# Kernel tuning notes

Measured on AMD Instinct MI355X. Metric: run time of the kernel, lower is better.

## Reference

```python
import jax, jax.numpy as jnp
import numpy as np

FEATURE_DIM = 512
HIDDEN_DIM = 512
N_HEADS = 8
HEAD_DIM = HIDDEN_DIM // N_HEADS
MAX_LEN = 5000
GAMMA = 0.5  # gaussian relative-position bias width
LN_EPS = 1e-5


def make_pe(d_model, max_len):
    # sinusoidal positional encoding buffer, as in PositionalEncoding.__init__
    pos = jnp.arange(max_len, dtype=jnp.float32)[:, None]
    div = jnp.exp(jnp.arange(0, d_model, 2, dtype=jnp.float32) * (-np.log(10000.0) / d_model))
    ang = pos * div  # [max_len, d_model/2]
    pe = jnp.zeros((max_len, d_model), dtype=jnp.float32)
    pe = pe.at[:, 0::2].set(jnp.sin(ang)).at[:, 1::2].set(jnp.cos(ang))
    return pe


def setup_inputs() -> dict:
    key = jax.random.key(0)
    k_x, k_q, k_k, k_v = jax.random.split(key, 4)
    xavier = np.sqrt(6.0 / (FEATURE_DIM + HEAD_DIM))  # xavier_uniform over last two dims
    return {
        "data_window": jax.random.normal(k_x, (1, 2048, FEATURE_DIM), dtype=jnp.float32),
        "W_query": jax.random.uniform(k_q, (N_HEADS, FEATURE_DIM, HEAD_DIM), jnp.float32, -xavier, xavier),
        "W_key": jax.random.uniform(k_k, (N_HEADS, FEATURE_DIM, HEAD_DIM), jnp.float32, -xavier, xavier),
        "W_value": jax.random.uniform(k_v, (N_HEADS, FEATURE_DIM, HEAD_DIM), jnp.float32, -xavier, xavier),
        "ln_gamma": jnp.ones((FEATURE_DIM,), dtype=jnp.float32),
        "ln_beta": jnp.zeros((FEATURE_DIM,), dtype=jnp.float32),
    }


def reference(data_window, W_query, W_key, W_value, ln_gamma, ln_beta):
    B, S, F = data_window.shape
    temperature = 1.0

    # LayerNorm over feature dim
    mu = jnp.mean(data_window, axis=-1, keepdims=True)
    var = jnp.mean(jnp.square(data_window - mu), axis=-1, keepdims=True)
    x = (data_window - mu) * jax.lax.rsqrt(var + LN_EPS) * ln_gamma + ln_beta

    # positional encoding, exactly as original: x + pe[:x.shape[0]] (requires B==1)
    pe = make_pe(FEATURE_DIM, MAX_LEN)
    x = x + pe[:B]  # [B,F] broadcasts over [B,S,F] only because B==1

    # per-head QKV projections, vectorized over heads
    Q = jnp.einsum('bsf,hfd->bhsd', x, W_query)
    K = jnp.einsum('bsf,hfd->bhsd', x, W_key)
    V = jnp.einsum('bsf,hfd->bhsd', x, W_value)

    scores = jnp.einsum('bhsd,bhtd->bhst', Q, K) / np.sqrt(HEAD_DIM)

    # gaussian relative-position bias: scale(=1) * exp(-gamma * (i-j)^2)
    p = jnp.arange(S, dtype=jnp.float32)
    rel = p[:, None] - p[None, :]
    bias = jnp.exp(-GAMMA * jnp.square(rel))  # [S,S]
    scores = (scores + bias[None, None]) / temperature
    # dropout on scores is identity in eval mode

    attn = jax.nn.softmax(scores, axis=-1)  # [B,H,S,S]
    head_out = jnp.einsum('bhst,bhtd->bhsd', attn, V)

    # concat heads along feature dim: [B,S,H*D]
    multi_head_output = head_out.transpose(0, 2, 1, 3).reshape(B, S, N_HEADS * HEAD_DIM)
    mean_weights = jnp.mean(attn, axis=1)  # [B,S,S]
    return multi_head_output, mean_weights
```

## Files before the change

kernel.cpp:

```cpp
#include <hip/hip_runtime.h>
#include <hip/hip_bf16.h>
#include <math.h>

#define S_LEN 2048
#define FDIM  512
#define NH    8
#define HD    64
#define MH_ELEMS (S_LEN * FDIM)
#define MEAN_ELEMS (S_LEN * S_LEN)

typedef _Float16 half_t;
typedef _Float16 half2v __attribute__((ext_vector_type(2)));
typedef _Float16 half4v __attribute__((ext_vector_type(4)));
typedef _Float16 half8v __attribute__((ext_vector_type(8)));
typedef float    float4v __attribute__((ext_vector_type(4)));
typedef int      int4v   __attribute__((ext_vector_type(4)));
typedef unsigned short ushort4v __attribute__((ext_vector_type(4)));

#define MFMA16(a, b, c) __builtin_amdgcn_mfma_f32_16x16x32_f16((a), (b), (c), 0, 0, 0)

static __device__ __forceinline__ unsigned short f2bf(float x) {
    union { __hip_bfloat16 b; unsigned short u; } cv;
    cv.b = __float2bfloat16(x);
    return cv.u;
}

__global__ __launch_bounds__(256) void prep_kernel(const float* __restrict__ x,
                                                   const float* __restrict__ gamma,
                                                   const float* __restrict__ beta,
                                                   const float* __restrict__ Wq,
                                                   const float* __restrict__ Wk,
                                                   const float* __restrict__ Wv,
                                                   half_t* __restrict__ xo,
                                                   half_t* __restrict__ WT) {
    const int tid = threadIdx.x;
    if (blockIdx.x < 2048) {
        const int row = blockIdx.x;
        const float2 v = ((const float2*)(x + (size_t)row * FDIM))[tid];
        float s = v.x + v.y;
        float q = v.x * v.x + v.y * v.y;
        #pragma unroll
        for (int off = 1; off < 64; off <<= 1) {
            s += __shfl_xor(s, off, 64);
            q += __shfl_xor(q, off, 64);
        }
        __shared__ float red[8];
        const int wave = tid >> 6;
        if ((tid & 63) == 0) { red[wave] = s; red[4 + wave] = q; }
        __syncthreads();
        s = red[0] + red[1] + red[2] + red[3];
        q = red[4] + red[5] + red[6] + red[7];
        const float mu  = s * (1.0f / FDIM);
        const float var = q * (1.0f / FDIM) - mu * mu;
        const float rstd = rsqrtf(var + 1e-5f);
        const int f0 = tid * 2, f1 = tid * 2 + 1;
        const float o0 = (v.x - mu) * rstd * gamma[f0] + beta[f0];
        const float o1 = (v.y - mu) * rstd * gamma[f1] + beta[f1] + 1.0f;
        half2v o; o.x = (half_t)o0; o.y = (half_t)o1;
        ((half2v*)(xo + (size_t)row * FDIM))[tid] = o;
    } else {
        const int idx = blockIdx.x - 2048;
        const int k0 = (idx & 7) * 64;
        const int h  = (idx >> 3) & 7;
        const int z  = idx >> 6;
        const float* W = ((z == 0) ? Wq : (z == 1) ? Wk : Wv) + (size_t)h * FDIM * HD;
        __shared__ float Ls[64][65];
        {
            const int kk = tid >> 2, dg = (tid & 3) * 16;
            #pragma unroll
            for (int j = 0; j < 4; ++j) {
                const float4 w = *(const float4*)(W + (size_t)(k0 + kk) * HD + dg + j * 4);
                Ls[kk][dg + j * 4 + 0] = w.x; Ls[kk][dg + j * 4 + 1] = w.y;
                Ls[kk][dg + j * 4 + 2] = w.z; Ls[kk][dg + j * 4 + 3] = w.w;
            }
        }
        __syncthreads();
        {
            const int d = tid >> 2, kg = (tid & 3) * 16;
            half8v t0, t1;
            #pragma unroll
            for (int j = 0; j < 8; ++j) t0[j] = (half_t)Ls[kg + j][d];
            #pragma unroll
            for (int j = 0; j < 8; ++j) t1[j] = (half_t)Ls[kg + 8 + j][d];
            half_t* dst = WT + ((size_t)(z * NH + h) * HD + d) * FDIM + k0 + kg;
            *(half8v*)dst = t0;
            *(half8v*)(dst + 8) = t1;
        }
    }
}

__global__ __launch_bounds__(256) void qkv_kernel(const half_t* __restrict__ xh,
                                                  const half_t* __restrict__ WT,
                                                  half_t* __restrict__ Qo,
                                                  half_t* __restrict__ Ko,
                                                  half_t* __restrict__ VTo) {
    const int ms0 = blockIdx.x * 128;
    const int h   = blockIdx.y, z = blockIdx.z;
    const half_t* Wt = WT + (size_t)(z * NH + h) * HD * FDIM;

    const int tid = threadIdx.x;
    const int wv = tid >> 6, lane = tid & 63;
    const int lo = lane & 15, qq = lane >> 4;

    float4v acc[2][4];
    #pragma unroll
    for (int rg = 0; rg < 2; ++rg)
        #pragma unroll
        for (int cg = 0; cg < 4; ++cg) acc[rg][cg] = (float4v){0.f, 0.f, 0.f, 0.f};

    const half_t* ar[2];
    ar[0] = xh + (size_t)(ms0 + wv * 32 + lo) * FDIM + qq * 8;
    ar[1] = ar[0] + 16 * FDIM;
    const half_t* wrow[4];
    #pragma unroll
    for (int cg = 0; cg < 4; ++cg) wrow[cg] = Wt + (size_t)(cg * 16 + lo) * FDIM + qq * 8;

    half8v a_c[2][2], b_c[4][2];
    #pragma unroll
    for (int rg = 0; rg < 2; ++rg) { a_c[rg][0] = *(const half8v*)(ar[rg]); a_c[rg][1] = *(const half8v*)(ar[rg] + 32); }
    #pragma unroll
    for (int cg = 0; cg < 4; ++cg) { b_c[cg][0] = *(const half8v*)(wrow[cg]); b_c[cg][1] = *(const half8v*)(wrow[cg] + 32); }

    for (int k0 = 0; k0 < FDIM; k0 += 64) {
        const int kn0 = (k0 + 64 < FDIM) ? k0 + 64 : 0;
        const int kn1 = (k0 + 96 < FDIM) ? k0 + 96 : 0;
        half8v a_n[2][2], b_n[4][2];
        #pragma unroll
        for (int rg = 0; rg < 2; ++rg) { a_n[rg][0] = *(const half8v*)(ar[rg] + kn0); a_n[rg][1] = *(const half8v*)(ar[rg] + kn1); }
        #pragma unroll
        for (int cg = 0; cg < 4; ++cg) { b_n[cg][0] = *(const half8v*)(wrow[cg] + kn0); b_n[cg][1] = *(const half8v*)(wrow[cg] + kn1); }
        #pragma unroll
        for (int kh = 0; kh < 2; ++kh)
            #pragma unroll
            for (int rg = 0; rg < 2; ++rg)
                #pragma unroll
                for (int cg = 0; cg < 4; ++cg)
                    acc[rg][cg] = MFMA16(a_c[rg][kh], b_c[cg][kh], acc[rg][cg]);
        #pragma unroll
        for (int rg = 0; rg < 2; ++rg) { a_c[rg][0] = a_n[rg][0]; a_c[rg][1] = a_n[rg][1]; }
        #pragma unroll
        for (int cg = 0; cg < 4; ++cg) { b_c[cg][0] = b_n[cg][0]; b_c[cg][1] = b_n[cg][1]; }
    }

    if (z < 2) {
        half_t* Co = ((z == 0) ? Qo : Ko) + (size_t)h * S_LEN * HD;
        #pragma unroll
        for (int rg = 0; rg < 2; ++rg)
            #pragma unroll
            for (int cg = 0; cg < 4; ++cg)
                #pragma unroll
                for (int r = 0; r < 4; ++r)
                    Co[(size_t)(ms0 + wv * 32 + rg * 16 + qq * 4 + r) * HD + cg * 16 + lo] =
                        (half_t)acc[rg][cg][r];
    } else {
        __shared__ float Ls[128][65];
        #pragma unroll
        for (int rg = 0; rg < 2; ++rg)
            #pragma unroll
            for (int cg = 0; cg < 4; ++cg)
                #pragma unroll
                for (int r = 0; r < 4; ++r)
                    Ls[wv * 32 + rg * 16 + qq * 4 + r][cg * 16 + lo] = acc[rg][cg][r];
        __syncthreads();
        const int d = tid & 63, sg = tid >> 6;
        half_t* dst = VTo + (size_t)(h * HD + d) * S_LEN + ms0 + sg * 32;
        #pragma unroll
        for (int c = 0; c < 4; ++c) {
            half8v t;
            #pragma unroll
            for (int j = 0; j < 8; ++j) t[j] = (half_t)Ls[sg * 32 + c * 8 + j][d];
            *(half8v*)(dst + c * 8) = t;
        }
    }
}

__global__ __launch_bounds__(256) void attn2_kernel(const half_t* __restrict__ Qw,
                                                    const half_t* __restrict__ Kw,
                                                    const half_t* __restrict__ VT,
                                                    unsigned short* __restrict__ Praw,
                                                    half_t* __restrict__ Op,
                                                    float* __restrict__ mp,
                                                    float* __restrict__ lp) {
    const int s0 = blockIdx.x * 32;
    const int h  = blockIdx.y;
    const int z  = blockIdx.z;
    const half_t* Qh = Qw + (size_t)h * S_LEN * HD;
    const half_t* Kh = Kw + (size_t)h * S_LEN * HD;
    const half_t* Vt = VT + (size_t)h * (size_t)HD * S_LEN;

    __shared__ float Osh[4][32][65];
    __shared__ float lsh[4][32];
    __shared__ float msh[4][32];

    const int tid = threadIdx.x;
    const int wv = tid >> 6, lane = tid & 63;
    const int lo = lane & 15, qq = lane >> 4;
    const int tb = z * 1024 + wv * 256;

    const half8v qA0 = *(const half8v*)(Qh + (size_t)(s0 + lo) * HD + qq * 8);
    const half8v qA1 = *(const half8v*)(Qh + (size_t)(s0 + lo) * HD + 32 + qq * 8);
    const half8v qB0 = *(const half8v*)(Qh + (size_t)(s0 + 16 + lo) * HD + qq * 8);
    const half8v qB1 = *(const half8v*)(Qh + (size_t)(s0 + 16 + lo) * HD + 32 + qq * 8);

    float4v accA[4], accB[4];
    #pragma unroll
    for (int dt = 0; dt < 4; ++dt) {
        accA[dt] = (float4v){0.f, 0.f, 0.f, 0.f};
        accB[dt] = (float4v){0.f, 0.f, 0.f, 0.f};
    }
    float mA = 0.f, mB = 0.f, lA = 0.f, lB = 0.f;

    const int srcLow  = lo + ((qq & 1) * 2) * 16;
    const int srcHigh = srcLow + 16;
    const bool sel1 = (qq >> 1) != 0;

    unsigned short* prA = Praw + ((size_t)h << 22) + (size_t)(s0 + lo) * S_LEN + qq * 4;
    unsigned short* prB = prA + 16 * S_LEN;

    half8v kc[4];
    {
        const half_t* kp0 = Kh + (size_t)(tb + lo) * HD;
        const half_t* kp1 = Kh + (size_t)(tb + 16 + lo) * HD;
        kc[0] = *(const half8v*)(kp0 + qq * 8);
        kc[1] = *(const half8v*)(kp0 + 32 + qq * 8);
        kc[2] = *(const half8v*)(kp1 + qq * 8);
        kc[3] = *(const half8v*)(kp1 + 32 + qq * 8);
    }

    for (int ps = 0; ps < 8; ++ps) {
        const int Tg  = tb + ps * 32;
        const int Tgn = tb + ((ps < 7) ? ps + 1 : ps) * 32;
        half8v kn[4], vc[4];
        {
            const half_t* kp0 = Kh + (size_t)(Tgn + lo) * HD;
            const half_t* kp1 = Kh + (size_t)(Tgn + 16 + lo) * HD;
            kn[0] = *(const half8v*)(kp0 + qq * 8);
            kn[1] = *(const half8v*)(kp0 + 32 + qq * 8);
            kn[2] = *(const half8v*)(kp1 + qq * 8);
            kn[3] = *(const half8v*)(kp1 + 32 + qq * 8);
            #pragma unroll
            for (int dt = 0; dt < 4; ++dt)
                vc[dt] = *(const half8v*)(Vt + (size_t)(dt * 16 + lo) * S_LEN + Tg + qq * 8);
        }
        float4v c0A = (float4v){0.f, 0.f, 0.f, 0.f};
        c0A = MFMA16(kc[0], qA0, c0A); c0A = MFMA16(kc[1], qA1, c0A);
        float4v c1A = (float4v){0.f, 0.f, 0.f, 0.f};
        c1A = MFMA16(kc[2], qA0, c1A); c1A = MFMA16(kc[3], qA1, c1A);
        float4v c0B = (float4v){0.f, 0.f, 0.f, 0.f};
        c0B = MFMA16(kc[0], qB0, c0B); c0B = MFMA16(kc[1], qB1, c0B);
        float4v c1B = (float4v){0.f, 0.f, 0.f, 0.f};
        c1B = MFMA16(kc[2], qB0, c1B); c1B = MFMA16(kc[3], qB1, c1B);

        const int dd0 = s0 - Tg;
        const bool nA0 = (dd0 > -40) && (dd0 < 40);
        const bool nA1 = (dd0 - 16 > -40) && (dd0 - 16 < 40);
        const bool nB0 = (dd0 + 16 > -40) && (dd0 + 16 < 40);
        const bool nB1 = nA0;
        float S0A[4], S1A[4], S0B[4], S1B[4];
        #pragma unroll
        for (int r = 0; r < 4; ++r) {
            const int t0 = Tg + qq * 4 + r, t1 = t0 + 16;
            float sa0 = c0A[r] * 0.125f;
            if (nA0) { const float d = (float)(s0 + lo - t0); sa0 += __expf(-0.5f * d * d); }
            float sa1 = c1A[r] * 0.125f;
            if (nA1) { const float d = (float)(s0 + lo - t1); sa1 += __expf(-0.5f * d * d); }
            float sb0 = c0B[r] * 0.125f;
            if (nB0) { const float d = (float)(s0 + 16 + lo - t0); sb0 += __expf(-0.5f * d * d); }
            float sb1 = c1B[r] * 0.125f;
            if (nB1) { const float d = (float)(s0 + 16 + lo - t1); sb1 += __expf(-0.5f * d * d); }
            S0A[r] = sa0; S1A[r] = sa1; S0B[r] = sb0; S1B[r] = sb1;
        }
        float smA = fmaxf(fmaxf(fmaxf(S0A[0], S0A[1]), fmaxf(S0A[2], S0A[3])),
                          fmaxf(fmaxf(S1A[0], S1A[1]), fmaxf(S1A[2], S1A[3])));
        float smB = fmaxf(fmaxf(fmaxf(S0B[0], S0B[1]), fmaxf(S0B[2], S0B[3])),
                          fmaxf(fmaxf(S1B[0], S1B[1]), fmaxf(S1B[2], S1B[3])));
        smA = fmaxf(smA, __shfl_xor(smA, 16, 64));
        smA = fmaxf(smA, __shfl_xor(smA, 32, 64));
        smB = fmaxf(smB, __shfl_xor(smB, 16, 64));
        smB = fmaxf(smB, __shfl_xor(smB, 32, 64));
        const float mnA = fmaxf(mA, smA), mnB = fmaxf(mB, smB);
        const float alA = __expf(mA - mnA), alB = __expf(mB - mnB);
        mA = mnA; mB = mnB;
        float E0A[4], E1A[4], E0B[4], E1B[4];
        float lsA = 0.f, lsB = 0.f;
        #pragma unroll
        for (int r = 0; r < 4; ++r) {
            E0A[r] = __expf(S0A[r] - mnA); E1A[r] = __expf(S1A[r] - mnA);
            E0B[r] = __expf(S0B[r] - mnB); E1B[r] = __expf(S1B[r] - mnB);
            lsA += E0A[r] + E1A[r];
            lsB += E0B[r] + E1B[r];
        }
        lA = lA * alA + lsA;
        lB = lB * alB + lsB;
        #pragma unroll
        for (int dt = 0; dt < 4; ++dt)
            #pragma unroll
            for (int i = 0; i < 4; ++i) { accA[dt][i] *= alA; accB[dt][i] *= alB; }

        {
            const float emA = __expf(mnA), emB = __expf(mnB);
            ushort4v e0a, e1a, e0b, e1b;
            #pragma unroll
            for (int r = 0; r < 4; ++r) {
                e0a[r] = f2bf(E0A[r] * emA); e1a[r] = f2bf(E1A[r] * emA);
                e0b[r] = f2bf(E0B[r] * emB); e1b[r] = f2bf(E1B[r] * emB);
            }
            *(ushort4v*)(prA + Tg)      = e0a;
            *(ushort4v*)(prA + Tg + 16) = e1a;
            *(ushort4v*)(prB + Tg)      = e0b;
            *(ushort4v*)(prB + Tg + 16) = e1b;
        }

        int pkA0, pkA1, pkA2, pkA3, pkB0, pkB1, pkB2, pkB3;
        {
            half2v p;
            p.x = (half_t)E0A[0]; p.y = (half_t)E0A[1]; pkA0 = __builtin_bit_cast(int, p);
            p.x = (half_t)E0A[2]; p.y = (half_t)E0A[3]; pkA1 = __builtin_bit_cast(int, p);
            p.x = (half_t)E1A[0]; p.y = (half_t)E1A[1]; pkA2 = __builtin_bit_cast(int, p);
            p.x = (half_t)E1A[2]; p.y = (half_t)E1A[3]; pkA3 = __builtin_bit_cast(int, p);
            p.x = (half_t)E0B[0]; p.y = (half_t)E0B[1]; pkB0 = __builtin_bit_cast(int, p);
            p.x = (half_t)E0B[2]; p.y = (half_t)E0B[3]; pkB1 = __builtin_bit_cast(int, p);
            p.x = (half_t)E1B[0]; p.y = (half_t)E1B[1]; pkB2 = __builtin_bit_cast(int, p);
            p.x = (half_t)E1B[2]; p.y = (half_t)E1B[3]; pkB3 = __builtin_bit_cast(int, p);
        }
        int4v biA, biB;
        {
            const int l0a = __shfl(pkA0, srcLow, 64),  l0b = __shfl(pkA2, srcLow, 64);
            const int l1a = __shfl(pkA1, srcLow, 64),  l1b = __shfl(pkA3, srcLow, 64);
            const int h0a = __shfl(pkA0, srcHigh, 64), h0b = __shfl(pkA2, srcHigh, 64);
            const int h1a = __shfl(pkA1, srcHigh, 64), h1b = __shfl(pkA3, srcHigh, 64);
            biA[0] = sel1 ? l0b : l0a;
            biA[1] = sel1 ? l1b : l1a;
            biA[2] = sel1 ? h0b : h0a;
            biA[3] = sel1 ? h1b : h1a;
        }
        {
            const int l0a = __shfl(pkB0, srcLow, 64),  l0b = __shfl(pkB2, srcLow, 64);
            const int l1a = __shfl(pkB1, srcLow, 64),  l1b = __shfl(pkB3, srcLow, 64);
            const int h0a = __shfl(pkB0, srcHigh, 64), h0b = __shfl(pkB2, srcHigh, 64);
            const int h1a = __shfl(pkB1, srcHigh, 64), h1b = __shfl(pkB3, srcHigh, 64);
            biB[0] = sel1 ? l0b : l0a;
            biB[1] = sel1 ? l1b : l1a;
            biB[2] = sel1 ? h0b : h0a;
            biB[3] = sel1 ? h1b : h1a;
        }
        const half8v bpA = __builtin_bit_cast(half8v, biA);
        const half8v bpB = __builtin_bit_cast(half8v, biB);
        #pragma unroll
        for (int dt = 0; dt < 4; ++dt) {
            accA[dt] = MFMA16(vc[dt], bpA, accA[dt]);
            accB[dt] = MFMA16(vc[dt], bpB, accB[dt]);
        }
        #pragma unroll
        for (int i = 0; i < 4; ++i) kc[i] = kn[i];
    }

    lA += __shfl_xor(lA, 16, 64); lA += __shfl_xor(lA, 32, 64);
    lB += __shfl_xor(lB, 16, 64); lB += __shfl_xor(lB, 32, 64);
    if (qq == 0) {
        lsh[wv][lo] = lA;      msh[wv][lo] = mA;
        lsh[wv][16 + lo] = lB; msh[wv][16 + lo] = mB;
    }
    #pragma unroll
    for (int dt = 0; dt < 4; ++dt)
        #pragma unroll
        for (int r = 0; r < 4; ++r) {
            Osh[wv][lo][dt * 16 + qq * 4 + r]      = accA[dt][r];
            Osh[wv][16 + lo][dt * 16 + qq * 4 + r] = accB[dt][r];
        }
    __syncthreads();

    #pragma unroll
    for (int p = 0; p < 2; ++p) {
        const int q = p * 16 + (tid >> 4), dg = tid & 15;
        const float m0 = msh[0][q], m1 = msh[1][q], m2 = msh[2][q], m3 = msh[3][q];
        const float M = fmaxf(fmaxf(m0, m1), fmaxf(m2, m3));
        const float f0 = __expf(m0 - M), f1 = __expf(m1 - M);
        const float f2 = __expf(m2 - M), f3 = __expf(m3 - M);
        const float L = lsh[0][q] * f0 + lsh[1][q] * f1 + lsh[2][q] * f2 + lsh[3][q] * f3;
        half4v o;
        #pragma unroll
        for (int i = 0; i < 4; ++i) {
            const float ov = Osh[0][q][dg * 4 + i] * f0 + Osh[1][q][dg * 4 + i] * f1 +
                             Osh[2][q][dg * 4 + i] * f2 + Osh[3][q][dg * 4 + i] * f3;
            o[i] = (half_t)ov;
        }
        const size_t pidx = (size_t)(z * NH + h) * S_LEN + s0 + q;
        *(half4v*)(Op + pidx * HD + dg * 4) = o;
        if (dg == 0) { mp[pidx] = M; lp[pidx] = L; }
    }
}

__global__ __launch_bounds__(256) void meanmerge_kernel(const half_t* __restrict__ Op,
                                                        const float* __restrict__ mp,
                                                        const float* __restrict__ lp,
                                                        const unsigned short* __restrict__ Praw,
                                                        float* __restrict__ out) {
    const int q = blockIdx.x;
    const int tid = threadIdx.x;
    __shared__ float lish[NH];
    {
        const int h = tid >> 5, t32 = tid & 31;
        const size_t i0 = (size_t)h * S_LEN + q;
        const size_t i1 = (size_t)(NH + h) * S_LEN + q;
        const float m0 = mp[i0], m1 = mp[i1];
        const float M = fmaxf(m0, m1);
        const float f0 = __expf(m0 - M), f1 = __expf(m1 - M);
        const float L = lp[i0] * f0 + lp[i1] * f1;
        const float inv = 1.0f / L;
        if (t32 == 0) lish[h] = __expf(-M) * inv;
        const int d = t32 * 2;
        const half2v o0 = *(const half2v*)(Op + i0 * HD + d);
        const half2v o1 = *(const half2v*)(Op + i1 * HD + d);
        float2 o;
        o.x = ((float)o0.x * f0 + (float)o1.x * f1) * inv;
        o.y = ((float)o0.y * f0 + (float)o1.y * f1) * inv;
        *(float2*)(out + (size_t)q * FDIM + h * HD + d) = o;
    }
    __syncthreads();
    {
        const int idx = tid * 8;
        float acc[8] = {0.f, 0.f, 0.f, 0.f, 0.f, 0.f, 0.f, 0.f};
        #pragma unroll
        for (int h = 0; h < NH; ++h) {
            const uint4 u = *(const uint4*)(Praw + ((size_t)h << 22) + (size_t)q * S_LEN + idx);
            const float li = lish[h];
            const unsigned int uu[4] = {u.x, u.y, u.z, u.w};
            #pragma unroll
            for (int j = 0; j < 4; ++j) {
                const float a = __builtin_bit_cast(float, uu[j] << 16);
                const float b = __builtin_bit_cast(float, uu[j] & 0xFFFF0000u);
                acc[2 * j]     += a * li;
                acc[2 * j + 1] += b * li;
            }
        }
        float* o = out + MH_ELEMS + (size_t)q * S_LEN + idx;
        *(float4*)o       = make_float4(acc[0] * 0.125f, acc[1] * 0.125f, acc[2] * 0.125f, acc[3] * 0.125f);
        *(float4*)(o + 4) = make_float4(acc[4] * 0.125f, acc[5] * 0.125f, acc[6] * 0.125f, acc[7] * 0.125f);
    }
}

extern "C" void kernel_launch(void* const* d_in, const int* in_sizes, int n_in,
                              void* d_out, int out_size, void* d_ws, size_t ws_size,
                              hipStream_t stream) {
    const float* x  = (const float*)d_in[0];
    const float* Wq = (const float*)d_in[1];
    const float* Wk = (const float*)d_in[2];
    const float* Wv = (const float*)d_in[3];
    const float* g  = (const float*)d_in[4];
    const float* b  = (const float*)d_in[5];
    float* out = (float*)d_out;
    char*  ws  = (char*)d_ws;

    half_t* Qh   = (half_t*)(ws);
    half_t* Kh   = (half_t*)(ws + (2ull  << 20));
    half_t* VT   = (half_t*)(ws + (4ull  << 20));
    half_t* xh   = (half_t*)(ws + (6ull  << 20));
    half_t* WT   = (half_t*)(ws + (8ull  << 20));
    half_t* Op   = (half_t*)(ws + (10ull << 20));
    float*  mp   = (float*) (ws + (14ull << 20));
    float*  lp   = (float*) (ws + (14ull << 20) + (128ull << 10));
    unsigned short* Praw = (unsigned short*)(ws + (16ull << 20));

    prep_kernel<<<2240, 256, 0, stream>>>(x, g, b, Wq, Wk, Wv, xh, WT);
    qkv_kernel<<<dim3(16, 8, 3), 256, 0, stream>>>(xh, WT, Qh, Kh, VT);
    attn2_kernel<<<dim3(64, 8, 2), 256, 0, stream>>>(Qh, Kh, VT, Praw, Op, mp, lp);
    meanmerge_kernel<<<S_LEN, 256, 0, stream>>>(Op, mp, lp, Praw, out);
}
```

Before: 157.5 us.

## Recompute attention probabilities in mean kernel instead of storing bf16 P matrix

The attention kernel no longer writes per-head unnormalized probabilities (8x2048x2048 bf16) to workspace. A new mean kernel recomputes QK^T per head with MFMA and turns each score into a normalized probability using the saved row max and log-sum. It applies the gaussian bias as a multiplicative exp(exp(-0.5 d^2)) factor, and only on tiles near the diagonal. This removes roughly 64MB of write plus read traffic in exchange for a second QK^T pass and extra exps, and the bias-by-tile shortcut depends on the bias vanishing in fp32 far from the diagonal.

```diff
diff --git a/kernel.cpp b/kernel.cpp
--- a/kernel.cpp
+++ b/kernel.cpp
@@ -15,15 +15,8 @@
 typedef _Float16 half8v __attribute__((ext_vector_type(8)));
 typedef float    float4v __attribute__((ext_vector_type(4)));
 typedef int      int4v   __attribute__((ext_vector_type(4)));
-typedef unsigned short ushort4v __attribute__((ext_vector_type(4)));
 
 #define MFMA16(a, b, c) __builtin_amdgcn_mfma_f32_16x16x32_f16((a), (b), (c), 0, 0, 0)
-
-static __device__ __forceinline__ unsigned short f2bf(float x) {
-    union { __hip_bfloat16 b; unsigned short u; } cv;
-    cv.b = __float2bfloat16(x);
-    return cv.u;
-}
 
 __global__ __launch_bounds__(256) void prep_kernel(const float* __restrict__ x,
                                                    const float* __restrict__ gamma,
@@ -177,7 +170,6 @@
 __global__ __launch_bounds__(256) void attn2_kernel(const half_t* __restrict__ Qw,
                                                     const half_t* __restrict__ Kw,
                                                     const half_t* __restrict__ VT,
-                                                    unsigned short* __restrict__ Praw,
                                                     half_t* __restrict__ Op,
                                                     float* __restrict__ mp,
                                                     float* __restrict__ lp) {
@@ -213,9 +205,6 @@
     const int srcLow  = lo + ((qq & 1) * 2) * 16;
     const int srcHigh = srcLow + 16;
     const bool sel1 = (qq >> 1) != 0;
-
-    unsigned short* prA = Praw + ((size_t)h << 22) + (size_t)(s0 + lo) * S_LEN + qq * 4;
-    unsigned short* prB = prA + 16 * S_LEN;
 
     half8v kc[4];
     {
@@ -297,20 +286,6 @@
             #pragma unroll
             for (int i = 0; i < 4; ++i) { accA[dt][i] *= alA; accB[dt][i] *= alB; }
 
-        {
-            const float emA = __expf(mnA), emB = __expf(mnB);
-            ushort4v e0a, e1a, e0b, e1b;
-            #pragma unroll
-            for (int r = 0; r < 4; ++r) {
-                e0a[r] = f2bf(E0A[r] * emA); e1a[r] = f2bf(E1A[r] * emA);
-                e0b[r] = f2bf(E0B[r] * emB); e1b[r] = f2bf(E1B[r] * emB);
-            }
-            *(ushort4v*)(prA + Tg)      = e0a;
-            *(ushort4v*)(prA + Tg + 16) = e1a;
-            *(ushort4v*)(prB + Tg)      = e0b;
-            *(ushort4v*)(prB + Tg + 16) = e1b;
-        }
-
         int pkA0, pkA1, pkA2, pkA3, pkB0, pkB1, pkB2, pkB3;
         {
             half2v p;
@@ -391,52 +366,124 @@
     }
 }
 
-__global__ __launch_bounds__(256) void meanmerge_kernel(const half_t* __restrict__ Op,
-                                                        const float* __restrict__ mp,
-                                                        const float* __restrict__ lp,
-                                                        const unsigned short* __restrict__ Praw,
-                                                        float* __restrict__ out) {
-    const int q = blockIdx.x;
+__global__ __launch_bounds__(256) void mean2_kernel(const half_t* __restrict__ Qw,
+                                                    const half_t* __restrict__ Kw,
+                                                    const half_t* __restrict__ Op,
+                                                    const float* __restrict__ mp,
+                                                    const float* __restrict__ lp,
+                                                    float* __restrict__ out) {
+    const int q0 = blockIdx.x * 32;
+    const int tbase = blockIdx.y * 128;
     const int tid = threadIdx.x;
-    __shared__ float lish[NH];
+
+    __shared__ float lnc[NH][32];
+    __shared__ float g0s[NH][32];
+    __shared__ float g1s[NH][32];
     {
-        const int h = tid >> 5, t32 = tid & 31;
-        const size_t i0 = (size_t)h * S_LEN + q;
-        const size_t i1 = (size_t)(NH + h) * S_LEN + q;
+        const int h = tid >> 5, qi = tid & 31;
+        const size_t i0 = (size_t)h * S_LEN + q0 + qi;
+        const size_t i1 = (size_t)(NH + h) * S_LEN + q0 + qi;
         const float m0 = mp[i0], m1 = mp[i1];
         const float M = fmaxf(m0, m1);
         const float f0 = __expf(m0 - M), f1 = __expf(m1 - M);
         const float L = lp[i0] * f0 + lp[i1] * f1;
         const float inv = 1.0f / L;
-        if (t32 == 0) lish[h] = __expf(-M) * inv;
-        const int d = t32 * 2;
-        const half2v o0 = *(const half2v*)(Op + i0 * HD + d);
-        const half2v o1 = *(const half2v*)(Op + i1 * HD + d);
-        float2 o;
-        o.x = ((float)o0.x * f0 + (float)o1.x * f1) * inv;
-        o.y = ((float)o0.y * f0 + (float)o1.y * f1) * inv;
-        *(float2*)(out + (size_t)q * FDIM + h * HD + d) = o;
+        lnc[h][qi] = -M - __logf(L);
+        g0s[h][qi] = f0 * inv;
+        g1s[h][qi] = f1 * inv;
     }
     __syncthreads();
-    {
-        const int idx = tid * 8;
-        float acc[8] = {0.f, 0.f, 0.f, 0.f, 0.f, 0.f, 0.f, 0.f};
+
+    const int wv = tid >> 6, lane = tid & 63;
+    const int lo = lane & 15, qq = lane >> 4;
+    const int t0 = tbase + wv * 32;
+
+    float4v macc[2][2];
+    #pragma unroll
+    for (int rg = 0; rg < 2; ++rg)
+        #pragma unroll
+        for (int tg = 0; tg < 2; ++tg) macc[rg][tg] = (float4v){0.f, 0.f, 0.f, 0.f};
+
+    const half_t* qp = Qw + (size_t)(q0 + lo) * HD + qq * 8;
+    const half_t* kp = Kw + (size_t)(t0 + lo) * HD + qq * 8;
+
+    #pragma unroll 2
+    for (int h = 0; h < NH; ++h) {
+        half8v a[2][2], b[2][2];
+        #pragma unroll
+        for (int rg = 0; rg < 2; ++rg) {
+            a[rg][0] = *(const half8v*)(qp + (size_t)rg * 16 * HD);
+            a[rg][1] = *(const half8v*)(qp + (size_t)rg * 16 * HD + 32);
+        }
+        #pragma unroll
+        for (int tg = 0; tg < 2; ++tg) {
+            b[tg][0] = *(const half8v*)(kp + (size_t)tg * 16 * HD);
+            b[tg][1] = *(const half8v*)(kp + (size_t)tg * 16 * HD + 32);
+        }
+        float4v sacc[2][2];
+        #pragma unroll
+        for (int rg = 0; rg < 2; ++rg)
+            #pragma unroll
+            for (int tg = 0; tg < 2; ++tg) sacc[rg][tg] = (float4v){0.f, 0.f, 0.f, 0.f};
+        #pragma unroll
+        for (int kh = 0; kh < 2; ++kh)
+            #pragma unroll
+            for (int rg = 0; rg < 2; ++rg)
+                #pragma unroll
+                for (int tg = 0; tg < 2; ++tg)
+                    sacc[rg][tg] = MFMA16(a[rg][kh], b[tg][kh], sacc[rg][tg]);
+
+        const float4v ln0 = *(const float4v*)&lnc[h][qq * 4];
+        const float4v ln1 = *(const float4v*)&lnc[h][16 + qq * 4];
+        #pragma unroll
+        for (int tg = 0; tg < 2; ++tg)
+            #pragma unroll
+            for (int r = 0; r < 4; ++r) {
+                macc[0][tg][r] += __expf(fmaf(sacc[0][tg][r], 0.125f, ln0[r]));
+                macc[1][tg][r] += __expf(fmaf(sacc[1][tg][r], 0.125f, ln1[r]));
+            }
+        qp += (size_t)S_LEN * HD;
+        kp += (size_t)S_LEN * HD;
+    }
+
+    const bool near = ((q0 + 31 - t0) > -40) && ((q0 - (t0 + 31)) < 40);
+    #pragma unroll
+    for (int rg = 0; rg < 2; ++rg)
+        #pragma unroll
+        for (int tg = 0; tg < 2; ++tg)
+            #pragma unroll
+            for (int r = 0; r < 4; ++r) {
+                const int qe = q0 + rg * 16 + qq * 4 + r;
+                const int te = t0 + tg * 16 + lo;
+                float w = macc[rg][tg][r] * 0.125f;
+                if (near) {
+                    const float d = (float)(qe - te);
+                    w *= __expf(__expf(-0.5f * d * d));
+                }
+                out[MH_ELEMS + (size_t)qe * S_LEN + te] = w;
+            }
+
+    if (blockIdx.y == 0) {
+        const int qi = tid >> 3, dg = (tid & 7) * 8;
+        const int q = q0 + qi;
         #pragma unroll
         for (int h = 0; h < NH; ++h) {
-            const uint4 u = *(const uint4*)(Praw + ((size_t)h << 22) + (size_t)q * S_LEN + idx);
-            const float li = lish[h];
-            const unsigned int uu[4] = {u.x, u.y, u.z, u.w};
-            #pragma unroll
-            for (int j = 0; j < 4; ++j) {
-                const float a = __builtin_bit_cast(float, uu[j] << 16);
-                const float b = __builtin_bit_cast(float, uu[j] & 0xFFFF0000u);
-                acc[2 * j]     += a * li;
-                acc[2 * j + 1] += b * li;
-            }
-        }
-        float* o = out + MH_ELEMS + (size_t)q * S_LEN + idx;
-        *(float4*)o       = make_float4(acc[0] * 0.125f, acc[1] * 0.125f, acc[2] * 0.125f, acc[3] * 0.125f);
-        *(float4*)(o + 4) = make_float4(acc[4] * 0.125f, acc[5] * 0.125f, acc[6] * 0.125f, acc[7] * 0.125f);
+            const half8v o0 = *(const half8v*)(Op + ((size_t)h * S_LEN + q) * HD + dg);
+            const half8v o1 = *(const half8v*)(Op + ((size_t)(NH + h) * S_LEN + q) * HD + dg);
+            const float a0 = g0s[h][qi], a1 = g1s[h][qi];
+            float4 r0, r1;
+            r0.x = (float)o0[0] * a0 + (float)o1[0] * a1;
+            r0.y = (float)o0[1] * a0 + (float)o1[1] * a1;
+            r0.z = (float)o0[2] * a0 + (float)o1[2] * a1;
+            r0.w = (float)o0[3] * a0 + (float)o1[3] * a1;
+            r1.x = (float)o0[4] * a0 + (float)o1[4] * a1;
+            r1.y = (float)o0[5] * a0 + (float)o1[5] * a1;
+            r1.z = (float)o0[6] * a0 + (float)o1[6] * a1;
+            r1.w = (float)o0[7] * a0 + (float)o1[7] * a1;
+            float* dst = out + (size_t)q * FDIM + h * HD + dg;
+            *(float4*)dst = r0;
+            *(float4*)(dst + 4) = r1;
+        }
     }
 }
 
@@ -460,10 +507,9 @@
     half_t* Op   = (half_t*)(ws + (10ull << 20));
     float*  mp   = (float*) (ws + (14ull << 20));
     float*  lp   = (float*) (ws + (14ull << 20) + (128ull << 10));
-    unsigned short* Praw = (unsigned short*)(ws + (16ull << 20));
 
     prep_kernel<<<2240, 256, 0, stream>>>(x, g, b, Wq, Wk, Wv, xh, WT);
     qkv_kernel<<<dim3(16, 8, 3), 256, 0, stream>>>(xh, WT, Qh, Kh, VT);
-    attn2_kernel<<<dim3(64, 8, 2), 256, 0, stream>>>(Qh, Kh, VT, Praw, Op, mp, lp);
-    meanmerge_kernel<<<S_LEN, 256, 0, stream>>>(Op, mp, lp, Praw, out);
+    attn2_kernel<<<dim3(64, 8, 2), 256, 0, stream>>>(Qh, Kh, VT, Op, mp, lp);
+    mean2_kernel<<<dim3(64, 16), 256, 0, stream>>>(Qh, Kh, Op, mp, lp, out);
 }
```

Result: slower. 166.1 us (+5.5%).
